# Performance work log

Hardware: AMD Instinct MI355X
Metric: run time of the kernel (lower is better)

The kernel has to match this reference:

```python
import jax, jax.numpy as jnp
import numpy as np

HIDDEN = 64
EMBED = 16
N_AGENTS = 1024
TRACK_LEN = 8


def setup_inputs() -> dict:
    key = jax.random.key(0)
    ks = jax.random.split(key, 6)
    s = lambda fan_in: 1.0 / np.sqrt(fan_in)
    return {
        "hidden_state": jax.random.normal(ks[0], (1, N_AGENTS, HIDDEN), jnp.float32),
        "group_track": jax.random.normal(ks[1], (N_AGENTS, TRACK_LEN, 2), jnp.float32),
        "W_e": jax.random.normal(ks[2], (2, EMBED), jnp.float32) * s(2),
        "b_e": jnp.zeros((EMBED,), jnp.float32),
        "W1": jax.random.normal(ks[3], (EMBED + HIDDEN, 2 * HIDDEN), jnp.float32) * s(EMBED + HIDDEN),
        "b1": jnp.zeros((2 * HIDDEN,), jnp.float32),
        "W2": jax.random.normal(ks[4], (2 * HIDDEN, HIDDEN), jnp.float32) * s(2 * HIDDEN),
        "b2": jnp.zeros((HIDDEN,), jnp.float32),
    }


def reference(hidden_state, group_track, W_e, b_e, W1, b1, W2, b2):
    n = group_track.shape[0]
    ends = group_track[:, -1, :]                       # [N, 2] end positions
    # rel[c, j] = end_j - end_c  (relative neighbor end pos per center agent)
    rel = ends[None, :, :] - ends[:, None, :]          # [N, N, 2]
    emb = rel @ W_e + b_e                              # [N, N, E]
    h = jnp.broadcast_to(hidden_state[0][None, :, :], (n, n, hidden_state.shape[-1]))
    x = jnp.concatenate([h, emb], axis=-1)             # [N, N, E+H] (hidden first, as in torch)
    y = jax.nn.relu(x @ W1 + b1)                       # [N, N, 2H]
    z = jax.nn.relu(y @ W2 + b2)                       # [N, N, H]
    pooled = z.max(axis=1)                             # max over neighbors -> [N, H]
    return pooled[None]                                # [1, N, H]
```

## Files before the change

### kernel.cpp

```cpp
#include <hip/hip_runtime.h>


#define N_AG 1024

typedef __attribute__((ext_vector_type(8))) short short8;
typedef __attribute__((ext_vector_type(4))) float floatx4;
typedef __attribute__((ext_vector_type(4))) unsigned int uintx4;

__device__ __forceinline__ unsigned short f2bf(float f) {
  unsigned u = __builtin_bit_cast(unsigned, f);
  u += 0x7FFFu + ((u >> 16) & 1u);
  return (unsigned short)(u >> 16);
}

__device__ __forceinline__ unsigned cvtpk_bf16(float y0, float y1) {
  unsigned r;
  asm("v_cvt_pk_bf16_f32 %0, %1, %2" : "=v"(r) : "v"(y0), "v"(y1));
  return r;
}

__global__ __launch_bounds__(128) void prep_all(
    const float* __restrict__ hidden,
    const float* __restrict__ track,
    const float* __restrict__ We,
    const float* __restrict__ be,
    const float* __restrict__ W1,
    const float* __restrict__ b1,
    const float* __restrict__ W2,
    unsigned short* __restrict__ Abf,
    float* __restrict__ M2f,
    unsigned short* __restrict__ W2T)
{
  int j = blockIdx.x;
  int k = threadIdx.x;
  __shared__ float hj[64];
  if (k < 64) hj[k] = hidden[j * 64 + k];
  __syncthreads();
  float e0 = track[j * 16 + 14];
  float e1 = track[j * 16 + 15];
  float m20 = 0.f, m21 = 0.f, cb = b1[k];
#pragma unroll
  for (int t = 0; t < 16; ++t) {
    float w1v = W1[(64 + t) * 128 + k];
    m20 += We[t] * w1v;
    m21 += We[16 + t] * w1v;
    cb  += be[t] * w1v;
  }
  float acc = e0 * m20 + e1 * m21 + cb;
#pragma unroll 16
  for (int t = 0; t < 64; ++t) acc += hj[t] * W1[t * 128 + k];
  __builtin_nontemporal_store(f2bf(acc), &Abf[j * 128 + k]);

  if (j == 0) {
    M2f[k]       = m20;
    M2f[128 + k] = m21;
  }
  if (j < 32) {
#pragma unroll
    for (int q = 0; q < 2; ++q) {
      int idx = j * 256 + q * 128 + k;
      int n = idx >> 7, c = idx & 127;
      W2T[n * 128 + c] = f2bf(W2[c * 64 + n]);
    }
  }
}

__global__ __launch_bounds__(256) void pool_main(
    const unsigned short* __restrict__ Abf,
    const float* __restrict__ M2f,
    const float* __restrict__ track,
    const unsigned short* __restrict__ W2T,
    const float* __restrict__ b2,
    float* __restrict__ out)
{
  const int i    = blockIdx.x;
  const int lane = threadIdx.x & 63;
  const int wave = threadIdx.x >> 6;
  const int m    = lane & 15;
  const int quad = lane >> 4;

  const unsigned short* Aptr = Abf + (wave * 16 + m) * 128 + quad * 8;
  uintx4 raw[4];
#pragma unroll
  for (int kk = 0; kk < 4; ++kk) raw[kk] = *(const uintx4*)(Aptr + kk * 32);

  const float e0 = track[i * 16 + 14];
  const float e1 = track[i * 16 + 15];
  float u[4][8];
#pragma unroll
  for (int kk = 0; kk < 4; ++kk) {
#pragma unroll
    for (int jj = 0; jj < 8; ++jj) {
      int kidx = kk * 32 + quad * 8 + jj;
      u[kk][jj] = e0 * M2f[kidx] + e1 * M2f[128 + kidx];
    }
  }

  short8 bfrag[4][4];
#pragma unroll
  for (int t = 0; t < 4; ++t)
#pragma unroll
    for (int kk = 0; kk < 4; ++kk)
      bfrag[t][kk] = *(const short8*)(W2T + (t * 16 + m) * 128 + kk * 32 + quad * 8);

  floatx4 mx[4];
#pragma unroll
  for (int t = 0; t < 4; ++t) mx[t] = (floatx4){-3e38f, -3e38f, -3e38f, -3e38f};

  for (int jt = wave; jt < 64; jt += 4) {
    Aptr += 4 * 16 * 128;
    const bool more = (jt + 4 < 64);
    uintx4 nxt[4];
    if (more) {
#pragma unroll
      for (int kk = 0; kk < 4; ++kk) nxt[kk] = *(const uintx4*)(Aptr + kk * 32);
    }

    uintx4 au[4];
#pragma unroll
    for (int kk = 0; kk < 4; ++kk) {
#pragma unroll
      for (int p = 0; p < 4; ++p) {
        unsigned w = raw[kk][p];
        float lo = __builtin_bit_cast(float, w << 16);
        float hi = __builtin_bit_cast(float, w & 0xFFFF0000u);
        float y0 = fmaxf(lo - u[kk][2 * p], 0.f);
        float y1 = fmaxf(hi - u[kk][2 * p + 1], 0.f);
        au[kk][p] = cvtpk_bf16(y0, y1);
      }
    }
#pragma unroll
    for (int t = 0; t < 4; ++t) {
      floatx4 acc = (floatx4){0.f, 0.f, 0.f, 0.f};
#pragma unroll
      for (int kk = 0; kk < 4; ++kk) {
        short8 af = __builtin_bit_cast(short8, au[kk]);
        acc = __builtin_amdgcn_mfma_f32_16x16x32_bf16(af, bfrag[t][kk], acc, 0, 0, 0);
      }
#pragma unroll
      for (int r = 0; r < 4; ++r) mx[t][r] = fmaxf(mx[t][r], acc[r]);
    }
    if (more) {
#pragma unroll
      for (int kk = 0; kk < 4; ++kk) raw[kk] = nxt[kk];
    }
  }

  float lm[4];
#pragma unroll
  for (int t = 0; t < 4; ++t) {
    lm[t] = fmaxf(fmaxf(mx[t][0], mx[t][1]), fmaxf(mx[t][2], mx[t][3]));
    lm[t] = fmaxf(lm[t], __shfl_xor(lm[t], 16, 64));
    lm[t] = fmaxf(lm[t], __shfl_xor(lm[t], 32, 64));
  }
  __shared__ float red[4][64];
  if (quad == 0) {
#pragma unroll
    for (int t = 0; t < 4; ++t) red[wave][t * 16 + m] = lm[t];
  }
  __syncthreads();
  if (threadIdx.x < 64) {
    int n = threadIdx.x;
    float v = fmaxf(fmaxf(red[0][n], red[1][n]), fmaxf(red[2][n], red[3][n]));
    v += b2[n];
    v = v > 0.f ? v : 0.f;
    out[i * 64 + n] = v;
  }
}

extern "C" void kernel_launch(void* const* d_in, const int* in_sizes, int n_in,
                              void* d_out, int out_size, void* d_ws, size_t ws_size,
                              hipStream_t stream) {
  const float* hidden = (const float*)d_in[0];
  const float* track  = (const float*)d_in[1];
  const float* We     = (const float*)d_in[2];
  const float* be     = (const float*)d_in[3];
  const float* W1     = (const float*)d_in[4];
  const float* b1     = (const float*)d_in[5];
  const float* W2     = (const float*)d_in[6];
  const float* b2     = (const float*)d_in[7];
  float* out = (float*)d_out;

  char* ws = (char*)d_ws;
  unsigned short* Abf = (unsigned short*)ws;
  float*          M2f = (float*)(ws + 262144);
  unsigned short* W2T = (unsigned short*)(ws + 263168);

  prep_all<<<N_AG, 128, 0, stream>>>(hidden, track, We, be, W1, b1, W2, Abf, M2f, W2T);
  pool_main<<<N_AG, 256, 0, stream>>>(Abf, M2f, track, W2T, b2, out);
}
```

Baseline: 109.8 us.

## Switch pooling GEMM to fp16 with packed sub-relu and split waves over outputs

Stores the precomputed first-layer activations and W2 in fp16 instead of bf16, so the subtract-and-ReLU runs as packed f16 ops (v_pk_add_f16/v_pk_max_f16) with no unpacking to fp32 and repacking. The second GEMM now uses the f16 MFMA. Waves are repartitioned so each handles half of the output columns over half the neighbours, which halves the B-fragments held per wave, and loads are double-buffered with a fully unrolled loop. Occupancy is hinted with launch_bounds(256,4). fp16 has a narrower range than bf16, so activations could lose precision or overflow, and each wave now redoes the sub-relu for twice as many neighbour tiles.

```diff
diff --git a/kernel.cpp b/kernel.cpp
--- a/kernel.cpp
+++ b/kernel.cpp
@@ -3,20 +3,20 @@
 
 #define N_AG 1024
 
-typedef __attribute__((ext_vector_type(8))) short short8;
+typedef __attribute__((ext_vector_type(8))) _Float16 half8;
 typedef __attribute__((ext_vector_type(4))) float floatx4;
 typedef __attribute__((ext_vector_type(4))) unsigned int uintx4;
 
-__device__ __forceinline__ unsigned short f2bf(float f) {
-  unsigned u = __builtin_bit_cast(unsigned, f);
-  u += 0x7FFFu + ((u >> 16) & 1u);
-  return (unsigned short)(u >> 16);
-}
-
-__device__ __forceinline__ unsigned cvtpk_bf16(float y0, float y1) {
-  unsigned r;
-  asm("v_cvt_pk_bf16_f32 %0, %1, %2" : "=v"(r) : "v"(y0), "v"(y1));
-  return r;
+__device__ __forceinline__ unsigned short f2h(float f) {
+  return __builtin_bit_cast(unsigned short, (_Float16)f);
+}
+
+__device__ __forceinline__ unsigned pk_sub_relu(unsigned a, unsigned u) {
+  unsigned d;
+  asm("v_pk_add_f16 %0, %1, %2 neg_lo:[0,1] neg_hi:[0,1]\n\t"
+      "v_pk_max_f16 %0, %0, 0"
+      : "=v"(d) : "v"(a), "v"(u));
+  return d;
 }
 
 __global__ __launch_bounds__(128) void prep_all(
@@ -27,7 +27,7 @@
     const float* __restrict__ W1,
     const float* __restrict__ b1,
     const float* __restrict__ W2,
-    unsigned short* __restrict__ Abf,
+    unsigned short* __restrict__ Ah,
     float* __restrict__ M2f,
     unsigned short* __restrict__ W2T)
 {
@@ -49,7 +49,7 @@
   float acc = e0 * m20 + e1 * m21 + cb;
 #pragma unroll 16
   for (int t = 0; t < 64; ++t) acc += hj[t] * W1[t * 128 + k];
-  __builtin_nontemporal_store(f2bf(acc), &Abf[j * 128 + k]);
+  __builtin_nontemporal_store(f2h(acc), &Ah[j * 128 + k]);
 
   if (j == 0) {
     M2f[k]       = m20;
@@ -60,13 +60,13 @@
     for (int q = 0; q < 2; ++q) {
       int idx = j * 256 + q * 128 + k;
       int n = idx >> 7, c = idx & 127;
-      W2T[n * 128 + c] = f2bf(W2[c * 64 + n]);
-    }
-  }
-}
-
-__global__ __launch_bounds__(256) void pool_main(
-    const unsigned short* __restrict__ Abf,
+      W2T[n * 128 + c] = f2h(W2[c * 64 + n]);
+    }
+  }
+}
+
+__global__ __launch_bounds__(256, 4) void pool_main(
+    const unsigned short* __restrict__ Ah,
     const float* __restrict__ M2f,
     const float* __restrict__ track,
     const unsigned short* __restrict__ W2T,
@@ -75,93 +75,110 @@
 {
   const int i    = blockIdx.x;
   const int lane = threadIdx.x & 63;
-  const int wave = threadIdx.x >> 6;
+  const int wv   = threadIdx.x >> 6;
+  const int wn   = wv & 1;
+  const int wj   = wv >> 1;
   const int m    = lane & 15;
   const int quad = lane >> 4;
 
-  const unsigned short* Aptr = Abf + (wave * 16 + m) * 128 + quad * 8;
-  uintx4 raw[4];
-#pragma unroll
-  for (int kk = 0; kk < 4; ++kk) raw[kk] = *(const uintx4*)(Aptr + kk * 32);
+  const int STEP = 2 * 16 * 128;
+  const unsigned short* Ap = Ah + (wj * 16 + m) * 128 + quad * 8;
+
+  uintx4 bufA[4], bufB[4];
+#pragma unroll
+  for (int kk = 0; kk < 4; ++kk) bufA[kk] = *(const uintx4*)(Ap + kk * 32);
+#pragma unroll
+  for (int kk = 0; kk < 4; ++kk) bufB[kk] = *(const uintx4*)(Ap + STEP + kk * 32);
 
   const float e0 = track[i * 16 + 14];
   const float e1 = track[i * 16 + 15];
-  float u[4][8];
+  unsigned upk[4][4];
 #pragma unroll
   for (int kk = 0; kk < 4; ++kk) {
 #pragma unroll
-    for (int jj = 0; jj < 8; ++jj) {
-      int kidx = kk * 32 + quad * 8 + jj;
-      u[kk][jj] = e0 * M2f[kidx] + e1 * M2f[128 + kidx];
-    }
-  }
-
-  short8 bfrag[4][4];
-#pragma unroll
-  for (int t = 0; t < 4; ++t)
+    for (int p = 0; p < 4; ++p) {
+      int k0 = kk * 32 + quad * 8 + 2 * p;
+      float a = e0 * M2f[k0]     + e1 * M2f[128 + k0];
+      float b = e0 * M2f[k0 + 1] + e1 * M2f[128 + k0 + 1];
+      upk[kk][p] = (unsigned)f2h(a) | ((unsigned)f2h(b) << 16);
+    }
+  }
+
+  half8 bfrag[2][4];
+#pragma unroll
+  for (int tb = 0; tb < 2; ++tb)
 #pragma unroll
     for (int kk = 0; kk < 4; ++kk)
-      bfrag[t][kk] = *(const short8*)(W2T + (t * 16 + m) * 128 + kk * 32 + quad * 8);
-
-  floatx4 mx[4];
-#pragma unroll
-  for (int t = 0; t < 4; ++t) mx[t] = (floatx4){-3e38f, -3e38f, -3e38f, -3e38f};
-
-  for (int jt = wave; jt < 64; jt += 4) {
-    Aptr += 4 * 16 * 128;
-    const bool more = (jt + 4 < 64);
-    uintx4 nxt[4];
-    if (more) {
-#pragma unroll
-      for (int kk = 0; kk < 4; ++kk) nxt[kk] = *(const uintx4*)(Aptr + kk * 32);
-    }
-
-    uintx4 au[4];
-#pragma unroll
-    for (int kk = 0; kk < 4; ++kk) {
-#pragma unroll
-      for (int p = 0; p < 4; ++p) {
-        unsigned w = raw[kk][p];
-        float lo = __builtin_bit_cast(float, w << 16);
-        float hi = __builtin_bit_cast(float, w & 0xFFFF0000u);
-        float y0 = fmaxf(lo - u[kk][2 * p], 0.f);
-        float y1 = fmaxf(hi - u[kk][2 * p + 1], 0.f);
-        au[kk][p] = cvtpk_bf16(y0, y1);
-      }
-    }
-#pragma unroll
-    for (int t = 0; t < 4; ++t) {
-      floatx4 acc = (floatx4){0.f, 0.f, 0.f, 0.f};
-#pragma unroll
-      for (int kk = 0; kk < 4; ++kk) {
-        short8 af = __builtin_bit_cast(short8, au[kk]);
-        acc = __builtin_amdgcn_mfma_f32_16x16x32_bf16(af, bfrag[t][kk], acc, 0, 0, 0);
-      }
-#pragma unroll
-      for (int r = 0; r < 4; ++r) mx[t][r] = fmaxf(mx[t][r], acc[r]);
-    }
-    if (more) {
-#pragma unroll
-      for (int kk = 0; kk < 4; ++kk) raw[kk] = nxt[kk];
-    }
-  }
-
-  float lm[4];
-#pragma unroll
-  for (int t = 0; t < 4; ++t) {
-    lm[t] = fmaxf(fmaxf(mx[t][0], mx[t][1]), fmaxf(mx[t][2], mx[t][3]));
-    lm[t] = fmaxf(lm[t], __shfl_xor(lm[t], 16, 64));
-    lm[t] = fmaxf(lm[t], __shfl_xor(lm[t], 32, 64));
-  }
-  __shared__ float red[4][64];
+      bfrag[tb][kk] = *(const half8*)(W2T + ((wn * 2 + tb) * 16 + m) * 128 + kk * 32 + quad * 8);
+
+  floatx4 mx[2];
+#pragma unroll
+  for (int tb = 0; tb < 2; ++tb) mx[tb] = (floatx4){-3e38f, -3e38f, -3e38f, -3e38f};
+
+#pragma unroll
+  for (int t = 0; t < 32; t += 2) {
+    {
+      uintx4 au[4];
+#pragma unroll
+      for (int kk = 0; kk < 4; ++kk)
+#pragma unroll
+        for (int p = 0; p < 4; ++p) au[kk][p] = pk_sub_relu(bufA[kk][p], upk[kk][p]);
+      if (t + 2 < 32) {
+        const unsigned short* p2 = Ap + (t + 2) * STEP;
+#pragma unroll
+        for (int kk = 0; kk < 4; ++kk) bufA[kk] = *(const uintx4*)(p2 + kk * 32);
+      }
+#pragma unroll
+      for (int tb = 0; tb < 2; ++tb) {
+        floatx4 acc = (floatx4){0.f, 0.f, 0.f, 0.f};
+#pragma unroll
+        for (int kk = 0; kk < 4; ++kk)
+          acc = __builtin_amdgcn_mfma_f32_16x16x32_f16(
+              __builtin_bit_cast(half8, au[kk]), bfrag[tb][kk], acc, 0, 0, 0);
+#pragma unroll
+        for (int r = 0; r < 4; ++r) mx[tb][r] = fmaxf(mx[tb][r], acc[r]);
+      }
+    }
+    {
+      uintx4 au[4];
+#pragma unroll
+      for (int kk = 0; kk < 4; ++kk)
+#pragma unroll
+        for (int p = 0; p < 4; ++p) au[kk][p] = pk_sub_relu(bufB[kk][p], upk[kk][p]);
+      if (t + 3 < 32) {
+        const unsigned short* p2 = Ap + (t + 3) * STEP;
+#pragma unroll
+        for (int kk = 0; kk < 4; ++kk) bufB[kk] = *(const uintx4*)(p2 + kk * 32);
+      }
+#pragma unroll
+      for (int tb = 0; tb < 2; ++tb) {
+        floatx4 acc = (floatx4){0.f, 0.f, 0.f, 0.f};
+#pragma unroll
+        for (int kk = 0; kk < 4; ++kk)
+          acc = __builtin_amdgcn_mfma_f32_16x16x32_f16(
+              __builtin_bit_cast(half8, au[kk]), bfrag[tb][kk], acc, 0, 0, 0);
+#pragma unroll
+        for (int r = 0; r < 4; ++r) mx[tb][r] = fmaxf(mx[tb][r], acc[r]);
+      }
+    }
+  }
+
+  float lm[2];
+#pragma unroll
+  for (int tb = 0; tb < 2; ++tb) {
+    lm[tb] = fmaxf(fmaxf(mx[tb][0], mx[tb][1]), fmaxf(mx[tb][2], mx[tb][3]));
+    lm[tb] = fmaxf(lm[tb], __shfl_xor(lm[tb], 16, 64));
+    lm[tb] = fmaxf(lm[tb], __shfl_xor(lm[tb], 32, 64));
+  }
+  __shared__ float red[2][64];
   if (quad == 0) {
 #pragma unroll
-    for (int t = 0; t < 4; ++t) red[wave][t * 16 + m] = lm[t];
+    for (int tb = 0; tb < 2; ++tb) red[wj][(wn * 2 + tb) * 16 + m] = lm[tb];
   }
   __syncthreads();
   if (threadIdx.x < 64) {
     int n = threadIdx.x;
-    float v = fmaxf(fmaxf(red[0][n], red[1][n]), fmaxf(red[2][n], red[3][n]));
+    float v = fmaxf(red[0][n], red[1][n]);
     v += b2[n];
     v = v > 0.f ? v : 0.f;
     out[i * 64 + n] = v;
@@ -182,10 +199,10 @@
   float* out = (float*)d_out;
 
   char* ws = (char*)d_ws;
-  unsigned short* Abf = (unsigned short*)ws;
+  unsigned short* Ah  = (unsigned short*)ws;
   float*          M2f = (float*)(ws + 262144);
   unsigned short* W2T = (unsigned short*)(ws + 263168);
 
-  prep_all<<<N_AG, 128, 0, stream>>>(hidden, track, We, be, W1, b1, W2, Abf, M2f, W2T);
-  pool_main<<<N_AG, 256, 0, stream>>>(Abf, M2f, track, W2T, b2, out);
-}
+  prep_all<<<N_AG, 128, 0, stream>>>(hidden, track, We, be, W1, b1, W2, Ah, M2f, W2T);
+  pool_main<<<N_AG, 256, 0, stream>>>(Ah, M2f, track, W2T, b2, out);
+}
```

New measurement: 140.6 us. 28.0% more time.
